# Optimization experiments

Hardware: AMD Instinct MI355X
Metric: run time of the kernel (lower is better)

Reference implementation:

```python
import jax, jax.numpy as jnp
import numpy as np

DIM = 256          # model dim
H = 8              # num heads
E = DIM // H       # head dim = 32
M = 32             # ball size
NB = 8192          # number of balls
N = NB * M         # total points = 262144
D3 = 3             # spatial dimensionality


def setup_inputs() -> dict:
    key = jax.random.key(0)
    ks = jax.random.split(key, 10)
    s = 1.0 / np.sqrt(DIM)
    return {
        "x": jax.random.normal(ks[0], (N, DIM), jnp.float32),
        "pos": jax.random.normal(ks[1], (N, D3), jnp.float32),
        "w_qkv": jax.random.normal(ks[2], (DIM, 3 * DIM), jnp.float32) * s,
        "b_qkv": jnp.zeros((3 * DIM,), jnp.float32),
        "w_pe": jax.random.normal(ks[3], (D3, DIM), jnp.float32) * (1.0 / np.sqrt(D3)),
        "b_pe": jnp.zeros((DIM,), jnp.float32),
        "w_proj": jax.random.normal(ks[4], (DIM, DIM), jnp.float32) * s,
        "b_proj": jnp.zeros((DIM,), jnp.float32),
        "sigma_att": -1.0 + 0.01 * jax.random.normal(ks[5], (1, H, 1, 1), jnp.float32),
    }


def reference(x, pos, w_qkv, b_qkv, w_pe, b_pe, w_proj, b_proj, sigma_att):
    n = x.shape[0] // M
    pos_b = pos.reshape(n, M, D3)                       # (n, m, 3)

    # eq. 9: relative position embedding wrt ball center
    centers = pos_b.mean(axis=1, keepdims=True)         # (n, 1, 3)
    rel = (pos_b - centers).reshape(n * M, D3)
    x = x + rel @ w_pe + b_pe                           # (N, DIM)

    # qkv projection; layout '(H E K)' with K fastest
    qkv = (x @ w_qkv + b_qkv).reshape(n, M, H, E, 3)
    q = jnp.transpose(qkv[..., 0], (0, 2, 1, 3))        # (n, H, m, E)
    k = jnp.transpose(qkv[..., 1], (0, 2, 1, 3))
    v = jnp.transpose(qkv[..., 2], (0, 2, 1, 3))

    # eq. 10: distance-based attention bias
    diff = pos_b[:, :, None, :] - pos_b[:, None, :, :]  # (n, m, m, 3)
    d2 = jnp.sum(diff * diff, axis=-1)
    dist = jnp.sqrt(jnp.maximum(d2, 1e-12))             # safe sqrt (grad at 0)
    bias = sigma_att * dist[:, None, :, :]              # (n, H, m, m)

    scale = 1.0 / np.sqrt(E)
    scores = jnp.einsum('nhme,nhke->nhmk', q, k) * scale + bias
    attn = jax.nn.softmax(scores, axis=-1)
    out = jnp.einsum('nhmk,nhke->nhme', attn, v)        # (n, H, m, E)
    out = jnp.transpose(out, (0, 2, 1, 3)).reshape(n * M, DIM)
    return out @ w_proj + b_proj
```

## Files before the change

kernel.cpp:

```cpp
#include <hip/hip_runtime.h>

#define NPTS   262144
#define NBALLS 8192
#define MSZ    32

typedef unsigned short u16;
typedef __attribute__((ext_vector_type(8))) unsigned short u16x8;
typedef __attribute__((ext_vector_type(4))) unsigned short u16x4;
typedef __attribute__((ext_vector_type(8))) __bf16 bf16x8;
typedef __attribute__((ext_vector_type(4))) float f32x4;
typedef __attribute__((ext_vector_type(2))) unsigned u32x2;

__device__ inline u16 f2bf(float f) {
    unsigned u = __builtin_bit_cast(unsigned, f);
    u += 0x7fffu + ((u >> 16) & 1u);
    return (u16)(u >> 16);
}

__device__ inline unsigned pk2(float lo, float hi) {
    return (unsigned)f2bf(lo) | ((unsigned)f2bf(hi) << 16);
}

__device__ inline f32x4 mfma16(u16x8 a, u16x8 b, f32x4 c) {
    return __builtin_amdgcn_mfma_f32_16x16x32_bf16(
        __builtin_bit_cast(bf16x8, a), __builtin_bit_cast(bf16x8, b), c, 0, 0, 0);
}

__device__ inline void gload_lds16(const u16* g, u16* l) {
    __builtin_amdgcn_global_load_lds(
        (const __attribute__((address_space(1))) void*)g,
        (__attribute__((address_space(3))) void*)l, 16, 0, 0);
}

__global__ __launch_bounds__(256) void k0_wprep(const float* __restrict__ w_qkv,
                                                const float* __restrict__ b_qkv,
                                                const float* __restrict__ w_proj,
                                                u16* __restrict__ wqkvT,
                                                u16* __restrict__ wpF,
                                                float* __restrict__ bq) {
    int idx = blockIdx.x * 256 + threadIdx.x;
    if (idx < 768 * 256) {
        int cp = idx >> 8, r = idx & 255;
        int k = cp >> 8, rem = cp & 255, h = rem >> 5, e = rem & 31;
        int orig = h * 96 + e * 3 + k;
        wqkvT[cp * 256 + r] = f2bf(w_qkv[r * 768 + orig]);
        if (r == 0) bq[cp] = b_qkv[orig];
    } else {
        int tid2 = idx - 768 * 256;
        int lane = tid2 & 63, ch = tid2 >> 6;
        int hk = ch & 7, gct = ch >> 3;
        int r15 = lane & 15, g4 = lane >> 4;
        u16x8 o;
#pragma unroll
        for (int j = 0; j < 8; ++j)
            o[j] = f2bf(w_proj[(size_t)(hk * 32 + g4 * 8 + j) * 256 + gct * 16 + r15]);
        *(u16x8*)&wpF[(size_t)tid2 * 8] = o;
    }
}

__global__ __launch_bounds__(512, 4) void k1_qkv(const float* __restrict__ x,
                                                 const float* __restrict__ pos,
                                                 const float* __restrict__ w_pe,
                                                 const float* __restrict__ b_pe,
                                                 const u16* __restrict__ wqkvT,
                                                 const float* __restrict__ bq,
                                                 u16* __restrict__ qkv2) {
    __shared__ __align__(16) u16 Bs[2][128 * 64];
    __shared__ float ps_s[384];
    __shared__ float ctr_s[4][3];
    __shared__ float rel_s[128][3];
    __shared__ float wpe_s[3][256];
    __shared__ float bpe_s[256];

    int id = blockIdx.x;
    int rt = (id >> 3) + (id & 7) * 256;
    int t = threadIdx.x;
    int lane = t & 63, wv = t >> 6;
    int r15 = lane & 15, g4 = lane >> 4;
    int wr = wv >> 1, wc = wv & 1;
    int rowbase = rt * 128;

    if (t < 384) ps_s[t] = pos[(size_t)rt * 384 + t];
    if (t < 256) bpe_s[t] = b_pe[t];
    for (int i = t; i < 768; i += 512) ((float*)wpe_s)[i] = w_pe[i];
    __syncthreads();
    if (t < 12) {
        int b = t / 3, m = t % 3;
        float s = 0.f;
#pragma unroll
        for (int j = 0; j < MSZ; ++j) s += ps_s[(b * 32 + j) * 3 + m];
        ctr_s[b][m] = s * (1.0f / MSZ);
    }
    __syncthreads();
    if (t < 384) {
        int p = t / 3, m = t % 3;
        ((float*)rel_s)[t] = ps_s[t] - ctr_s[p >> 5][m];
    }
#pragma unroll
    for (int i = 0; i < 2; ++i) {
        int c = i * 512 + t;
        int row = c >> 3, sg = c & 7;
        gload_lds16(&wqkvT[(size_t)row * 256 + (sg ^ (row & 7)) * 8], &Bs[0][c * 8]);
    }
    __syncthreads();

    u16* Ast = &Bs[1][0];
    u16x8 af[2][8];
#pragma unroll
    for (int kt = 0; kt < 4; ++kt) {
#pragma unroll
        for (int i = 0; i < 2; ++i) {
            int c = i * 512 + t;
            int row = c >> 3, g = c & 7;
            int kk0 = kt * 64 + g * 8;
            float4 xa = *(const float4*)&x[(size_t)(rowbase + row) * 256 + kk0];
            float4 xb = *(const float4*)&x[(size_t)(rowbase + row) * 256 + kk0 + 4];
            float r0 = rel_s[row][0], r1 = rel_s[row][1], r2 = rel_s[row][2];
            u16x8 o;
#pragma unroll
            for (int m = 0; m < 8; ++m) {
                float xv = (m < 4) ? ((const float*)&xa)[m] : ((const float*)&xb)[m - 4];
                float v = fmaf(r0, wpe_s[0][kk0 + m],
                          fmaf(r1, wpe_s[1][kk0 + m],
                          fmaf(r2, wpe_s[2][kk0 + m], xv))) + bpe_s[kk0 + m];
                o[m] = f2bf(v);
            }
            *(u16x8*)&Ast[(row * 8 + (g ^ (row & 7))) * 8] = o;
        }
        __syncthreads();
#pragma unroll
        for (int ks = 0; ks < 2; ++ks)
#pragma unroll
            for (int i = 0; i < 2; ++i) {
                int R = wr * 32 + i * 16 + r15;
                af[i][2 * kt + ks] =
                    *(const u16x8*)&Ast[R * 64 + (((ks * 4 + g4) ^ (R & 7)) * 8)];
            }
        __syncthreads();
    }

    f32x4 acc[4][2];
#pragma unroll
    for (int j = 0; j < 4; ++j)
#pragma unroll
        for (int i = 0; i < 2; ++i) acc[j][i] = (f32x4){0.f, 0.f, 0.f, 0.f};

    const int ball = rt * 4 + wr;
#pragma unroll
    for (int ct = 0; ct < 6; ++ct) {
#pragma unroll
        for (int kt = 0; kt < 4; ++kt) {
            int cur = kt & 1;
            if (kt < 3 || ct < 5) {
                int nct = (kt < 3) ? ct : ct + 1;
                int nkt = (kt < 3) ? kt + 1 : 0;
#pragma unroll
                for (int i = 0; i < 2; ++i) {
                    int c = i * 512 + t;
                    int row = c >> 3, sg = c & 7;
                    gload_lds16(&wqkvT[(size_t)(nct * 128 + row) * 256 + nkt * 64 + (sg ^ (row & 7)) * 8],
                                &Bs[cur ^ 1][c * 8]);
                }
            }
#pragma unroll
            for (int ks = 0; ks < 2; ++ks) {
                u16x8 b[4];
#pragma unroll
                for (int j = 0; j < 4; ++j) {
                    int C = wc * 64 + j * 16 + r15;
                    b[j] = *(const u16x8*)&Bs[cur][C * 64 + (((ks * 4 + g4) ^ (C & 7)) * 8)];
                }
#pragma unroll
                for (int j = 0; j < 4; ++j)
#pragma unroll
                    for (int i = 0; i < 2; ++i)
                        acc[j][i] = mfma16(b[j], af[i][2 * kt + ks], acc[j][i]);
            }
            if (kt == 3) {
#pragma unroll
                for (int j = 0; j < 4; ++j) {
                    int cp0 = ct * 128 + wc * 64 + j * 16 + g4 * 4;
                    float4 bias = *(const float4*)&bq[cp0];
                    int mat = cp0 >> 8, rem = cp0 & 255, h = rem >> 5, e0 = rem & 31;
                    size_t base = (size_t)ball * 24576 + mat * 8192 + h * 1024 + e0;
#pragma unroll
                    for (int i = 0; i < 2; ++i) {
                        int point = i * 16 + r15;
                        unsigned lo = pk2(acc[j][i][0] + bias.x, acc[j][i][1] + bias.y);
                        unsigned hi = pk2(acc[j][i][2] + bias.z, acc[j][i][3] + bias.w);
                        *(u32x2*)&qkv2[base + point * 32] = (u32x2){lo, hi};
                        acc[j][i] = (f32x4){0.f, 0.f, 0.f, 0.f};
                    }
                }
            }
            __syncthreads();
        }
    }
}

__global__ __launch_bounds__(256) void k23_attnproj(const float* __restrict__ pos,
                                                    const float* __restrict__ sigma,
                                                    const u16* __restrict__ qkv2,
                                                    const u16* __restrict__ wpF,
                                                    const float* __restrict__ bp,
                                                    float* __restrict__ out) {
    int ball = blockIdx.x, t = threadIdx.x;
    __shared__ float ps[MSZ][3];
    __shared__ float dist_s[MSZ][33];
    __shared__ __align__(16) u16 V_s[MSZ][256];
    __shared__ __align__(16) u16 P_s[4][MSZ][40];
    __shared__ __align__(16) u16 ao_s[MSZ][264];

    const size_t ballbase = (size_t)ball * 24576;

    if (t < MSZ * 3) ((float*)ps)[t] = pos[(size_t)ball * (MSZ * 3) + t];
    __syncthreads();
    for (int p = t; p < 1024; p += 256) {
        int m = p >> 5, k = p & 31;
        float dx = ps[m][0] - ps[k][0], dy = ps[m][1] - ps[k][1], dz = ps[m][2] - ps[k][2];
        dist_s[m][k] = sqrtf(fmaxf(dx * dx + dy * dy + dz * dz, 1e-12f));
    }
#pragma unroll
    for (int i = 0; i < 4; ++i) {
        int c = i * 256 + t;
        int h = c >> 7, wi = c & 127;
        int point = wi >> 2, g4w = wi & 3;
        int col8 = h * 32 + g4w * 8;
        int cs = col8 ^ (((point >> 3) & 3) << 4);
        *(u16x8*)&V_s[point][cs] = *(const u16x8*)&qkv2[ballbase + 16384 + (size_t)c * 8];
    }
    __syncthreads();

    int lane = t & 63, wv = t >> 6;
    int r15 = lane & 15, g4 = lane >> 4;
    const float scale = 0.17677669529663687f;

#pragma unroll
    for (int hh = 0; hh < 2; ++hh) {
        int h = wv * 2 + hh;
        float sig = sigma[h];
        u16x8 aq[2], bk[2];
#pragma unroll
        for (int i = 0; i < 2; ++i) {
            aq[i] = *(const u16x8*)&qkv2[ballbase + h * 1024 + (size_t)(i * 16 + r15) * 32 + g4 * 8];
            bk[i] = *(const u16x8*)&qkv2[ballbase + 8192 + h * 1024 + (size_t)(i * 16 + r15) * 32 + g4 * 8];
        }
        f32x4 s[2][2];
#pragma unroll
        for (int i = 0; i < 2; ++i)
#pragma unroll
            for (int j = 0; j < 2; ++j) s[i][j] = (f32x4){0.f, 0.f, 0.f, 0.f};
#pragma unroll
        for (int i = 0; i < 2; ++i)
#pragma unroll
            for (int j = 0; j < 2; ++j)
                s[i][j] = mfma16(aq[i], bk[j], s[i][j]);

#pragma unroll
        for (int i = 0; i < 2; ++i) {
#pragma unroll
            for (int r = 0; r < 4; ++r) {
                int row = i * 16 + g4 * 4 + r;
                float v0 = s[i][0][r] * scale + sig * dist_s[row][r15];
                float v1 = s[i][1][r] * scale + sig * dist_s[row][16 + r15];
                float m = fmaxf(v0, v1);
                m = fmaxf(m, __shfl_xor(m, 1));
                m = fmaxf(m, __shfl_xor(m, 2));
                m = fmaxf(m, __shfl_xor(m, 4));
                m = fmaxf(m, __shfl_xor(m, 8));
                float e0 = __expf(v0 - m), e1 = __expf(v1 - m);
                float su = e0 + e1;
                su += __shfl_xor(su, 1);
                su += __shfl_xor(su, 2);
                su += __shfl_xor(su, 4);
                su += __shfl_xor(su, 8);
                float rin = 1.0f / su;
                P_s[wv][row][r15]      = f2bf(e0 * rin);
                P_s[wv][row][16 + r15] = f2bf(e1 * rin);
            }
        }
        u16x8 pa[2];
#pragma unroll
        for (int i = 0; i < 2; ++i)
            pa[i] = *(const u16x8*)&P_s[wv][i * 16 + r15][g4 * 8];
        u16x8 bv[2];
#pragma unroll
        for (int j = 0; j < 2; ++j) {
#pragma unroll
            for (int jj = 0; jj < 8; ++jj) {
                int kp = g4 * 8 + jj;
                int colv = h * 32 + j * 16 + r15;
                bv[j][jj] = V_s[kp][colv ^ (((kp >> 3) & 3) << 4)];
            }
        }
        f32x4 o[2][2];
#pragma unroll
        for (int i = 0; i < 2; ++i)
#pragma unroll
            for (int j = 0; j < 2; ++j) o[i][j] = (f32x4){0.f, 0.f, 0.f, 0.f};
#pragma unroll
        for (int i = 0; i < 2; ++i)
#pragma unroll
            for (int j = 0; j < 2; ++j)
                o[i][j] = mfma16(pa[i], bv[j], o[i][j]);
#pragma unroll
        for (int i = 0; i < 2; ++i)
#pragma unroll
            for (int j = 0; j < 2; ++j)
#pragma unroll
                for (int r = 0; r < 4; ++r) {
                    int row = i * 16 + g4 * 4 + r;
                    int col = h * 32 + j * 16 + r15;
                    ao_s[row][col] = f2bf(o[i][j][r]);
                }
    }
    __syncthreads();

    f32x4 pacc[4][2];
#pragma unroll
    for (int tt = 0; tt < 4; ++tt)
#pragma unroll
        for (int i = 0; i < 2; ++i) pacc[tt][i] = (f32x4){0.f, 0.f, 0.f, 0.f};
#pragma unroll
    for (int hk = 0; hk < 8; ++hk) {
        u16x8 apj[2];
#pragma unroll
        for (int i = 0; i < 2; ++i)
            apj[i] = *(const u16x8*)&ao_s[i * 16 + r15][hk * 32 + g4 * 8];
#pragma unroll
        for (int tt = 0; tt < 4; ++tt) {
            int gct = wv * 4 + tt;
            u16x8 b = *(const u16x8*)&wpF[(size_t)((gct * 8 + hk) * 64 + lane) * 8];
            pacc[tt][0] = mfma16(apj[0], b, pacc[tt][0]);
            pacc[tt][1] = mfma16(apj[1], b, pacc[tt][1]);
        }
    }
#pragma unroll
    for (int tt = 0; tt < 4; ++tt) {
        int ct = (wv * 4 + tt) * 16;
        float bb = bp[ct + r15];
#pragma unroll
        for (int i = 0; i < 2; ++i)
#pragma unroll
            for (int r = 0; r < 4; ++r) {
                int row = ball * MSZ + i * 16 + g4 * 4 + r;
                out[(size_t)row * 256 + ct + r15] = pacc[tt][i][r] + bb;
            }
    }
}

extern "C" void kernel_launch(void* const* d_in, const int* in_sizes, int n_in,
                              void* d_out, int out_size, void* d_ws, size_t ws_size,
                              hipStream_t stream) {
    (void)in_sizes; (void)n_in; (void)out_size; (void)ws_size;
    const float* x      = (const float*)d_in[0];
    const float* pos    = (const float*)d_in[1];
    const float* w_qkv  = (const float*)d_in[2];
    const float* b_qkv  = (const float*)d_in[3];
    const float* w_pe   = (const float*)d_in[4];
    const float* b_pe   = (const float*)d_in[5];
    const float* w_proj = (const float*)d_in[6];
    const float* b_proj = (const float*)d_in[7];
    const float* sigma  = (const float*)d_in[8];
    float* out = (float*)d_out;

    u16* qkv2   = (u16*)d_ws;
    u16* wqkvT  = qkv2 + (size_t)NPTS * 768;
    u16* wpF    = wqkvT + 768 * 256;
    float* bq   = (float*)(wpF + 65536);

    k0_wprep<<<800, 256, 0, stream>>>(w_qkv, b_qkv, w_proj, wqkvT, wpF, bq);
    k1_qkv<<<2048, 512, 0, stream>>>(x, pos, w_pe, b_pe, wqkvT, bq, qkv2);
    k23_attnproj<<<NBALLS, 256, 0, stream>>>(pos, sigma, qkv2, wpF, b_proj, out);
}
```

Before: 421.1 us.

## Fuse per-head attention into QKV GEMM kernel, keep qkv in shared memory

Reorders the QKV weight columns per head so the QKV GEMM kernel produces one head's q, k and v at a time into shared memory, then immediately computes that head's attention for its ball. The bf16 qkv tensor (768 columns per point) no longer round-trips through global memory; only the 256-column attention output goes to a separate projection kernel. The cost is a smaller per-step N tile (96 columns), more barriers per head, only half of the warps doing the softmax write, and more shared memory per block, which may reduce occupancy.

Result: slower. 520.4 us (+23.6%).

```diff
diff --git a/kernel.cpp b/kernel.cpp
--- a/kernel.cpp
+++ b/kernel.cpp
@@ -6,7 +6,6 @@
 
 typedef unsigned short u16;
 typedef __attribute__((ext_vector_type(8))) unsigned short u16x8;
-typedef __attribute__((ext_vector_type(4))) unsigned short u16x4;
 typedef __attribute__((ext_vector_type(8))) __bf16 bf16x8;
 typedef __attribute__((ext_vector_type(4))) float f32x4;
 typedef __attribute__((ext_vector_type(2))) unsigned u32x2;
@@ -35,16 +34,16 @@
 __global__ __launch_bounds__(256) void k0_wprep(const float* __restrict__ w_qkv,
                                                 const float* __restrict__ b_qkv,
                                                 const float* __restrict__ w_proj,
-                                                u16* __restrict__ wqkvT,
+                                                u16* __restrict__ wqkvT2,
                                                 u16* __restrict__ wpF,
-                                                float* __restrict__ bq) {
+                                                float* __restrict__ bq2) {
     int idx = blockIdx.x * 256 + threadIdx.x;
     if (idx < 768 * 256) {
         int cp = idx >> 8, r = idx & 255;
-        int k = cp >> 8, rem = cp & 255, h = rem >> 5, e = rem & 31;
-        int orig = h * 96 + e * 3 + k;
-        wqkvT[cp * 256 + r] = f2bf(w_qkv[r * 768 + orig]);
-        if (r == 0) bq[cp] = b_qkv[orig];
+        int h = cp / 96, rem = cp % 96, mat = rem >> 5, e = rem & 31;
+        int orig = h * 96 + e * 3 + mat;
+        wqkvT2[cp * 256 + r] = f2bf(w_qkv[r * 768 + orig]);
+        if (r == 0) bq2[cp] = b_qkv[orig];
     } else {
         int tid2 = idx - 768 * 256;
         int lane = tid2 & 63, ch = tid2 >> 6;
@@ -58,19 +57,26 @@
     }
 }
 
-__global__ __launch_bounds__(512, 4) void k1_qkv(const float* __restrict__ x,
-                                                 const float* __restrict__ pos,
-                                                 const float* __restrict__ w_pe,
-                                                 const float* __restrict__ b_pe,
-                                                 const u16* __restrict__ wqkvT,
-                                                 const float* __restrict__ bq,
-                                                 u16* __restrict__ qkv2) {
-    __shared__ __align__(16) u16 Bs[2][128 * 64];
-    __shared__ float ps_s[384];
-    __shared__ float ctr_s[4][3];
-    __shared__ float rel_s[128][3];
-    __shared__ float wpe_s[3][256];
-    __shared__ float bpe_s[256];
+__global__ __launch_bounds__(512, 4) void k1_fused(const float* __restrict__ x,
+                                                   const float* __restrict__ pos,
+                                                   const float* __restrict__ w_pe,
+                                                   const float* __restrict__ b_pe,
+                                                   const u16* __restrict__ wqkvT2,
+                                                   const float* __restrict__ bq2,
+                                                   const float* __restrict__ sigma,
+                                                   u16* __restrict__ ao) {
+    __shared__ __align__(16) u16 Bs2[2][96 * 64];
+    __shared__ __align__(16) u16 qkvh[4][3][MSZ][32];
+    __shared__ float dist_s[4][MSZ][32];
+    __shared__ __align__(16) char upool[10240];
+
+    float* ps_s  = (float*)upool;
+    float* ctr_s = ps_s + 384;
+    float* rel_s = ctr_s + 12;
+    float* wpe_s = rel_s + 384;
+    float* bpe_s = wpe_s + 768;
+    typedef u16 (*PsT)[MSZ][40];
+    PsT P_s = (PsT)upool;
 
     int id = blockIdx.x;
     int rt = (id >> 3) + (id & 7) * 256;
@@ -79,32 +85,43 @@
     int r15 = lane & 15, g4 = lane >> 4;
     int wr = wv >> 1, wc = wv & 1;
     int rowbase = rt * 128;
+    const int ball_g = rt * 4 + wr;
+    const float scale = 0.17677669529663687f;
 
     if (t < 384) ps_s[t] = pos[(size_t)rt * 384 + t];
     if (t < 256) bpe_s[t] = b_pe[t];
-    for (int i = t; i < 768; i += 512) ((float*)wpe_s)[i] = w_pe[i];
+    for (int i = t; i < 768; i += 512) wpe_s[i] = w_pe[i];
+    {
+        int c = t, row = c >> 3, sg = c & 7;
+        gload_lds16(&wqkvT2[(size_t)row * 256 + (sg ^ (row & 7)) * 8], &Bs2[0][c * 8]);
+        if (t < 256) {
+            int c2 = 512 + t, row2 = c2 >> 3, sg2 = c2 & 7;
+            gload_lds16(&wqkvT2[(size_t)row2 * 256 + (sg2 ^ (row2 & 7)) * 8], &Bs2[0][c2 * 8]);
+        }
+    }
     __syncthreads();
     if (t < 12) {
         int b = t / 3, m = t % 3;
         float s = 0.f;
 #pragma unroll
         for (int j = 0; j < MSZ; ++j) s += ps_s[(b * 32 + j) * 3 + m];
-        ctr_s[b][m] = s * (1.0f / MSZ);
+        ctr_s[b * 3 + m] = s * (1.0f / MSZ);
     }
     __syncthreads();
     if (t < 384) {
         int p = t / 3, m = t % 3;
-        ((float*)rel_s)[t] = ps_s[t] - ctr_s[p >> 5][m];
-    }
-#pragma unroll
-    for (int i = 0; i < 2; ++i) {
-        int c = i * 512 + t;
-        int row = c >> 3, sg = c & 7;
-        gload_lds16(&wqkvT[(size_t)row * 256 + (sg ^ (row & 7)) * 8], &Bs[0][c * 8]);
+        rel_s[t] = ps_s[t] - ctr_s[(p >> 5) * 3 + m];
+    }
+    for (int idx2 = t; idx2 < 4096; idx2 += 512) {
+        int b = idx2 >> 10, m = (idx2 >> 5) & 31, kk = idx2 & 31;
+        float dx = ps_s[(b * 32 + m) * 3 + 0] - ps_s[(b * 32 + kk) * 3 + 0];
+        float dy = ps_s[(b * 32 + m) * 3 + 1] - ps_s[(b * 32 + kk) * 3 + 1];
+        float dz = ps_s[(b * 32 + m) * 3 + 2] - ps_s[(b * 32 + kk) * 3 + 2];
+        dist_s[b][m][kk] = sqrtf(fmaxf(dx * dx + dy * dy + dz * dz, 1e-12f));
     }
     __syncthreads();
 
-    u16* Ast = &Bs[1][0];
+    u16* Ast = &qkvh[0][0][0][0];
     u16x8 af[2][8];
 #pragma unroll
     for (int kt = 0; kt < 4; ++kt) {
@@ -115,14 +132,14 @@
             int kk0 = kt * 64 + g * 8;
             float4 xa = *(const float4*)&x[(size_t)(rowbase + row) * 256 + kk0];
             float4 xb = *(const float4*)&x[(size_t)(rowbase + row) * 256 + kk0 + 4];
-            float r0 = rel_s[row][0], r1 = rel_s[row][1], r2 = rel_s[row][2];
+            float r0 = rel_s[row * 3 + 0], r1 = rel_s[row * 3 + 1], r2 = rel_s[row * 3 + 2];
             u16x8 o;
 #pragma unroll
             for (int m = 0; m < 8; ++m) {
                 float xv = (m < 4) ? ((const float*)&xa)[m] : ((const float*)&xb)[m - 4];
-                float v = fmaf(r0, wpe_s[0][kk0 + m],
-                          fmaf(r1, wpe_s[1][kk0 + m],
-                          fmaf(r2, wpe_s[2][kk0 + m], xv))) + bpe_s[kk0 + m];
+                float v = fmaf(r0, wpe_s[0 * 256 + kk0 + m],
+                          fmaf(r1, wpe_s[1 * 256 + kk0 + m],
+                          fmaf(r2, wpe_s[2 * 256 + kk0 + m], xv))) + bpe_s[kk0 + m];
                 o[m] = f2bf(v);
             }
             *(u16x8*)&Ast[(row * 8 + (g ^ (row & 7))) * 8] = o;
@@ -139,130 +156,83 @@
         __syncthreads();
     }
 
-    f32x4 acc[4][2];
-#pragma unroll
-    for (int j = 0; j < 4; ++j)
+    f32x4 acc[3][2];
+#pragma unroll
+    for (int j = 0; j < 3; ++j)
 #pragma unroll
         for (int i = 0; i < 2; ++i) acc[j][i] = (f32x4){0.f, 0.f, 0.f, 0.f};
 
-    const int ball = rt * 4 + wr;
-#pragma unroll
-    for (int ct = 0; ct < 6; ++ct) {
+    for (int hd = 0; hd < 8; ++hd) {
 #pragma unroll
         for (int kt = 0; kt < 4; ++kt) {
             int cur = kt & 1;
-            if (kt < 3 || ct < 5) {
-                int nct = (kt < 3) ? ct : ct + 1;
-                int nkt = (kt < 3) ? kt + 1 : 0;
-#pragma unroll
-                for (int i = 0; i < 2; ++i) {
-                    int c = i * 512 + t;
-                    int row = c >> 3, sg = c & 7;
-                    gload_lds16(&wqkvT[(size_t)(nct * 128 + row) * 256 + nkt * 64 + (sg ^ (row & 7)) * 8],
-                                &Bs[cur ^ 1][c * 8]);
+            if (hd * 4 + kt < 31) {
+                int nhd = (kt == 3) ? hd + 1 : hd;
+                int nkt = (kt + 1) & 3;
+                int c = t, row = c >> 3, sg = c & 7;
+                gload_lds16(&wqkvT2[(size_t)(nhd * 96 + row) * 256 + nkt * 64 + (sg ^ (row & 7)) * 8],
+                            &Bs2[cur ^ 1][c * 8]);
+                if (t < 256) {
+                    int c2 = 512 + t, row2 = c2 >> 3, sg2 = c2 & 7;
+                    gload_lds16(&wqkvT2[(size_t)(nhd * 96 + row2) * 256 + nkt * 64 + (sg2 ^ (row2 & 7)) * 8],
+                                &Bs2[cur ^ 1][c2 * 8]);
                 }
             }
 #pragma unroll
             for (int ks = 0; ks < 2; ++ks) {
-                u16x8 b[4];
-#pragma unroll
-                for (int j = 0; j < 4; ++j) {
-                    int C = wc * 64 + j * 16 + r15;
-                    b[j] = *(const u16x8*)&Bs[cur][C * 64 + (((ks * 4 + g4) ^ (C & 7)) * 8)];
+                u16x8 b[3];
+#pragma unroll
+                for (int j = 0; j < 3; ++j) {
+                    int C = wc * 48 + j * 16 + r15;
+                    b[j] = *(const u16x8*)&Bs2[cur][C * 64 + (((ks * 4 + g4) ^ (C & 7)) * 8)];
                 }
 #pragma unroll
-                for (int j = 0; j < 4; ++j)
+                for (int j = 0; j < 3; ++j)
 #pragma unroll
                     for (int i = 0; i < 2; ++i)
                         acc[j][i] = mfma16(b[j], af[i][2 * kt + ks], acc[j][i]);
             }
             if (kt == 3) {
 #pragma unroll
-                for (int j = 0; j < 4; ++j) {
-                    int cp0 = ct * 128 + wc * 64 + j * 16 + g4 * 4;
-                    float4 bias = *(const float4*)&bq[cp0];
-                    int mat = cp0 >> 8, rem = cp0 & 255, h = rem >> 5, e0 = rem & 31;
-                    size_t base = (size_t)ball * 24576 + mat * 8192 + h * 1024 + e0;
+                for (int j = 0; j < 3; ++j) {
+                    int cp0 = wc * 48 + j * 16 + g4 * 4;
+                    float4 bias = *(const float4*)&bq2[hd * 96 + cp0];
+                    int mat = cp0 >> 5, e0 = cp0 & 31;
 #pragma unroll
                     for (int i = 0; i < 2; ++i) {
                         int point = i * 16 + r15;
                         unsigned lo = pk2(acc[j][i][0] + bias.x, acc[j][i][1] + bias.y);
                         unsigned hi = pk2(acc[j][i][2] + bias.z, acc[j][i][3] + bias.w);
-                        *(u32x2*)&qkv2[base + point * 32] = (u32x2){lo, hi};
+                        int ed = (mat == 2) ? (e0 ^ (((point >> 3) & 1) << 4)) : e0;
+                        *(u32x2*)&qkvh[wr][mat][point][ed] = (u32x2){lo, hi};
                         acc[j][i] = (f32x4){0.f, 0.f, 0.f, 0.f};
                     }
                 }
             }
             __syncthreads();
         }
-    }
-}
-
-__global__ __launch_bounds__(256) void k23_attnproj(const float* __restrict__ pos,
-                                                    const float* __restrict__ sigma,
-                                                    const u16* __restrict__ qkv2,
-                                                    const u16* __restrict__ wpF,
-                                                    const float* __restrict__ bp,
-                                                    float* __restrict__ out) {
-    int ball = blockIdx.x, t = threadIdx.x;
-    __shared__ float ps[MSZ][3];
-    __shared__ float dist_s[MSZ][33];
-    __shared__ __align__(16) u16 V_s[MSZ][256];
-    __shared__ __align__(16) u16 P_s[4][MSZ][40];
-    __shared__ __align__(16) u16 ao_s[MSZ][264];
-
-    const size_t ballbase = (size_t)ball * 24576;
-
-    if (t < MSZ * 3) ((float*)ps)[t] = pos[(size_t)ball * (MSZ * 3) + t];
-    __syncthreads();
-    for (int p = t; p < 1024; p += 256) {
-        int m = p >> 5, k = p & 31;
-        float dx = ps[m][0] - ps[k][0], dy = ps[m][1] - ps[k][1], dz = ps[m][2] - ps[k][2];
-        dist_s[m][k] = sqrtf(fmaxf(dx * dx + dy * dy + dz * dz, 1e-12f));
-    }
-#pragma unroll
-    for (int i = 0; i < 4; ++i) {
-        int c = i * 256 + t;
-        int h = c >> 7, wi = c & 127;
-        int point = wi >> 2, g4w = wi & 3;
-        int col8 = h * 32 + g4w * 8;
-        int cs = col8 ^ (((point >> 3) & 3) << 4);
-        *(u16x8*)&V_s[point][cs] = *(const u16x8*)&qkv2[ballbase + 16384 + (size_t)c * 8];
-    }
-    __syncthreads();
-
-    int lane = t & 63, wv = t >> 6;
-    int r15 = lane & 15, g4 = lane >> 4;
-    const float scale = 0.17677669529663687f;
-
-#pragma unroll
-    for (int hh = 0; hh < 2; ++hh) {
-        int h = wv * 2 + hh;
-        float sig = sigma[h];
+
+        float sig = sigma[hd];
         u16x8 aq[2], bk[2];
 #pragma unroll
         for (int i = 0; i < 2; ++i) {
-            aq[i] = *(const u16x8*)&qkv2[ballbase + h * 1024 + (size_t)(i * 16 + r15) * 32 + g4 * 8];
-            bk[i] = *(const u16x8*)&qkv2[ballbase + 8192 + h * 1024 + (size_t)(i * 16 + r15) * 32 + g4 * 8];
+            aq[i] = *(const u16x8*)&qkvh[wr][0][i * 16 + r15][g4 * 8];
+            bk[i] = *(const u16x8*)&qkvh[wr][1][i * 16 + r15][g4 * 8];
         }
         f32x4 s[2][2];
 #pragma unroll
         for (int i = 0; i < 2; ++i)
 #pragma unroll
-            for (int j = 0; j < 2; ++j) s[i][j] = (f32x4){0.f, 0.f, 0.f, 0.f};
-#pragma unroll
-        for (int i = 0; i < 2; ++i)
-#pragma unroll
             for (int j = 0; j < 2; ++j)
-                s[i][j] = mfma16(aq[i], bk[j], s[i][j]);
+                s[i][j] = mfma16(aq[i], bk[j], (f32x4){0.f, 0.f, 0.f, 0.f});
 
 #pragma unroll
         for (int i = 0; i < 2; ++i) {
 #pragma unroll
             for (int r = 0; r < 4; ++r) {
                 int row = i * 16 + g4 * 4 + r;
-                float v0 = s[i][0][r] * scale + sig * dist_s[row][r15];
-                float v1 = s[i][1][r] * scale + sig * dist_s[row][16 + r15];
+                float v0 = s[i][0][r] * scale + sig * dist_s[wr][row][r15];
+                float v1 = s[i][1][r] * scale + sig * dist_s[wr][row][16 + r15];
                 float m = fmaxf(v0, v1);
                 m = fmaxf(m, __shfl_xor(m, 1));
                 m = fmaxf(m, __shfl_xor(m, 2));
@@ -275,46 +245,46 @@
                 su += __shfl_xor(su, 4);
                 su += __shfl_xor(su, 8);
                 float rin = 1.0f / su;
-                P_s[wv][row][r15]      = f2bf(e0 * rin);
-                P_s[wv][row][16 + r15] = f2bf(e1 * rin);
-            }
-        }
+                if (wc == 0) {
+                    P_s[wr][row][r15]      = f2bf(e0 * rin);
+                    P_s[wr][row][16 + r15] = f2bf(e1 * rin);
+                }
+            }
+        }
+        __syncthreads();
+
         u16x8 pa[2];
 #pragma unroll
         for (int i = 0; i < 2; ++i)
-            pa[i] = *(const u16x8*)&P_s[wv][i * 16 + r15][g4 * 8];
-        u16x8 bv[2];
-#pragma unroll
-        for (int j = 0; j < 2; ++j) {
-#pragma unroll
-            for (int jj = 0; jj < 8; ++jj) {
-                int kp = g4 * 8 + jj;
-                int colv = h * 32 + j * 16 + r15;
-                bv[j][jj] = V_s[kp][colv ^ (((kp >> 3) & 3) << 4)];
-            }
-        }
-        f32x4 o[2][2];
-#pragma unroll
-        for (int i = 0; i < 2; ++i)
-#pragma unroll
-            for (int j = 0; j < 2; ++j) o[i][j] = (f32x4){0.f, 0.f, 0.f, 0.f};
-#pragma unroll
-        for (int i = 0; i < 2; ++i)
-#pragma unroll
-            for (int j = 0; j < 2; ++j)
-                o[i][j] = mfma16(pa[i], bv[j], o[i][j]);
-#pragma unroll
-        for (int i = 0; i < 2; ++i)
-#pragma unroll
-            for (int j = 0; j < 2; ++j)
-#pragma unroll
-                for (int r = 0; r < 4; ++r) {
-                    int row = i * 16 + g4 * 4 + r;
-                    int col = h * 32 + j * 16 + r15;
-                    ao_s[row][col] = f2bf(o[i][j][r]);
-                }
-    }
-    __syncthreads();
+            pa[i] = *(const u16x8*)&P_s[wr][i * 16 + r15][g4 * 8];
+        u16x8 bv;
+#pragma unroll
+        for (int jj = 0; jj < 8; ++jj) {
+            int kp = g4 * 8 + jj;
+            int ev = (wc * 16 + r15) ^ (((kp >> 3) & 1) << 4);
+            bv[jj] = qkvh[wr][2][kp][ev];
+        }
+#pragma unroll
+        for (int i = 0; i < 2; ++i) {
+            f32x4 o = mfma16(bv, pa[i], (f32x4){0.f, 0.f, 0.f, 0.f});
+            int point = i * 16 + r15;
+            int e0 = wc * 16 + g4 * 4;
+            unsigned lo = pk2(o[0], o[1]);
+            unsigned hi = pk2(o[2], o[3]);
+            *(u32x2*)&ao[(size_t)(ball_g * 32 + point) * 256 + hd * 32 + e0] = (u32x2){lo, hi};
+        }
+        __syncthreads();
+    }
+}
+
+__global__ __launch_bounds__(256) void k2_proj(const u16* __restrict__ ao,
+                                               const u16* __restrict__ wpF,
+                                               const float* __restrict__ bp,
+                                               float* __restrict__ out) {
+    int ball = blockIdx.x, t = threadIdx.x;
+    int lane = t & 63, wv = t >> 6;
+    int r15 = lane & 15, g4 = lane >> 4;
+    const size_t rowb = (size_t)ball * 32;
 
     f32x4 pacc[4][2];
 #pragma unroll
@@ -326,7 +296,7 @@
         u16x8 apj[2];
 #pragma unroll
         for (int i = 0; i < 2; ++i)
-            apj[i] = *(const u16x8*)&ao_s[i * 16 + r15][hk * 32 + g4 * 8];
+            apj[i] = *(const u16x8*)&ao[(rowb + i * 16 + r15) * 256 + hk * 32 + g4 * 8];
 #pragma unroll
         for (int tt = 0; tt < 4; ++tt) {
             int gct = wv * 4 + tt;
@@ -343,8 +313,8 @@
         for (int i = 0; i < 2; ++i)
 #pragma unroll
             for (int r = 0; r < 4; ++r) {
-                int row = ball * MSZ + i * 16 + g4 * 4 + r;
-                out[(size_t)row * 256 + ct + r15] = pacc[tt][i][r] + bb;
+                size_t row = rowb + i * 16 + g4 * 4 + r;
+                out[row * 256 + ct + r15] = pacc[tt][i][r] + bb;
             }
     }
 }
@@ -364,12 +334,12 @@
     const float* sigma  = (const float*)d_in[8];
     float* out = (float*)d_out;
 
-    u16* qkv2   = (u16*)d_ws;
-    u16* wqkvT  = qkv2 + (size_t)NPTS * 768;
-    u16* wpF    = wqkvT + 768 * 256;
-    float* bq   = (float*)(wpF + 65536);
-
-    k0_wprep<<<800, 256, 0, stream>>>(w_qkv, b_qkv, w_proj, wqkvT, wpF, bq);
-    k1_qkv<<<2048, 512, 0, stream>>>(x, pos, w_pe, b_pe, wqkvT, bq, qkv2);
-    k23_attnproj<<<NBALLS, 256, 0, stream>>>(pos, sigma, qkv2, wpF, b_proj, out);
-}
+    u16* ao      = (u16*)d_ws;
+    u16* wqkvT2  = ao + (size_t)NPTS * 256;
+    u16* wpF     = wqkvT2 + 768 * 256;
+    float* bq2   = (float*)(wpF + 65536);
+
+    k0_wprep<<<800, 256, 0, stream>>>(w_qkv, b_qkv, w_proj, wqkvT2, wpF, bq2);
+    k1_fused<<<2048, 512, 0, stream>>>(x, pos, w_pe, b_pe, wqkvT2, bq2, sigma, ao);
+    k2_proj<<<NBALLS, 256, 0, stream>>>(ao, wpF, b_proj, out);
+}
```
